# Performance work log

Hardware: AMD Instinct MI355X
Metric: run time of the kernel (lower is better)

## Reference

```python
import jax, jax.numpy as jnp
import numpy as np

B, N0, D0 = 256, 64, 128
N1, D1 = 64, 128


def setup_inputs() -> dict:
    key = jax.random.key(0)
    k1, k2 = jax.random.split(key)
    x = jax.random.normal(k1, (B, N0, D0), dtype=jnp.float32)
    # kaiming_normal_ (fan_in mode): fan_in = N0 * D0 * D1 for a [N1,N0,D0,D1] tensor
    std = np.sqrt(2.0 / (N0 * D0 * D1)).astype(np.float32)
    W = jax.random.normal(k2, (N1, N0, D0, D1), dtype=jnp.float32) * std
    b = jnp.zeros((N1, N0, 1), dtype=jnp.float32)
    return {"x": x, "W": W, "b": b}


def reference(x, W, b):
    u = jnp.einsum('bji,kjiz->bkjz', x, W)  # [B, N1, N0, D1]
    # c[b, n1, i] = sum_{k,j} u[b,n1,i,j] * u[b,n1,k,j] = u[b,n1,i,:] . sum_k u[b,n1,k,:]
    s = jnp.sum(u, axis=-2)                      # [B, N1, D1]
    c = jnp.einsum('bkjz,bkz->bkj', u, s)        # [B, N1, N0]
    c = c[..., None] / jnp.sqrt(jnp.asarray(u.shape[-1], dtype=u.dtype))
    c = jax.nn.softmax(c, axis=1)                # softmax over N1 (absolute axis 1)
    c = c + b
    return jnp.sum(u * c, axis=-2)               # [B, N1, D1]
```

## Files before the change

kernel.cpp:

```cpp
#include <hip/hip_runtime.h>
#include <hip/hip_bf16.h>
#include <cstdint>


#define BB 256
#define NN0 64
#define DD0 128
#define NN1 64
#define DD1 128

typedef __attribute__((ext_vector_type(8))) short bf16x8;
typedef __attribute__((ext_vector_type(4))) float f32x4;
typedef __attribute__((ext_vector_type(4))) ushort u16x4;

__device__ __forceinline__ ushort f2bf(float f) {
  uint32_t b = __float_as_uint(f);
  b += 0x7FFFu + ((b >> 16) & 1u);
  return (ushort)(b >> 16);
}
__device__ __forceinline__ float bf2f(ushort h) {
  return __uint_as_float(((uint32_t)h) << 16);
}

__device__ __forceinline__ void gld_lds16(const void* g, void* l) {
  __builtin_amdgcn_global_load_lds(
      (const __attribute__((address_space(1))) void*)g,
      (__attribute__((address_space(3))) void*)l, 16, 0, 0);
}

__device__ __forceinline__ void bar_lgkm() {
  asm volatile("s_waitcnt lgkmcnt(0)" ::: "memory");
  __builtin_amdgcn_s_barrier();
  __builtin_amdgcn_sched_barrier(0);
}

__global__ __launch_bounds__(512) void px_cvt(
    const float* __restrict__ x, ushort* __restrict__ xbf)
{
  int i = blockIdx.x * 512 + threadIdx.x;
  const f32x4* src = reinterpret_cast<const f32x4*>(x) + i;
  f32x4 v = __builtin_nontemporal_load(src);
  ushort4 h;
  h.x = f2bf(v.x); h.y = f2bf(v.y); h.z = f2bf(v.z); h.w = f2bf(v.w);
  *reinterpret_cast<ushort4*>(xbf + (size_t)i * 4) = h;
}

__global__ __launch_bounds__(512, 4) void k1_gemm(
    const ushort* __restrict__ xbf, const float* __restrict__ W,
    ushort* __restrict__ u)
{
  __shared__ __align__(16) char lds[81920];
  char* Alds = lds;
  char* Bl[2] = { lds + 65536, lds + 73728 };

  const int q = blockIdx.x;
  const int local = q >> 3;
  const int n0 = (q & 7) * 8 + (local >> 6);
  const int n1 = local & 63;
  const int t = threadIdx.x;
  const int lane = t & 63, wave = t >> 6;
  const int wm = wave >> 1, wn = wave & 1;

  const ushort* xb = xbf + n0 * DD0;
  const float* Wb = W + ((size_t)n1 * NN0 + n0) * (DD0 * DD1);
  ushort* ub = u + ((size_t)n1 * 8192 + (size_t)n0 * 128);

  f32x4 acc[4][4];
#pragma unroll
  for (int a = 0; a < 4; ++a)
#pragma unroll
    for (int b = 0; b < 4; ++b) acc[a][b] = {0.f, 0.f, 0.f, 0.f};

  const int gd1 = t & 127, gkc = t >> 7;
  const int bbyte = (gd1 * 64 + gkc * 16) ^ ((gd1 & 3) << 4) ^ (((gd1 >> 2) & 1) << 6);
  float w0[8], w1[8];

#define LOADW(hh, ks)                                                         \
  {                                                                           \
    _Pragma("unroll")                                                         \
    for (int j = 0; j < 8; ++j)                                               \
      hh[j] = __builtin_nontemporal_load(                                     \
          Wb + (size_t)((ks) * 32 + gkc * 8 + j) * 128 + gd1);                \
  }
#define PACKB(bi, hh)                                                         \
  {                                                                           \
    uint32_t p0 = (uint32_t)f2bf(hh[0]) | ((uint32_t)f2bf(hh[1]) << 16);      \
    uint32_t p1 = (uint32_t)f2bf(hh[2]) | ((uint32_t)f2bf(hh[3]) << 16);      \
    uint32_t p2 = (uint32_t)f2bf(hh[4]) | ((uint32_t)f2bf(hh[5]) << 16);      \
    uint32_t p3 = (uint32_t)f2bf(hh[6]) | ((uint32_t)f2bf(hh[7]) << 16);      \
    *reinterpret_cast<uint4*>(Bl[bi] + bbyte) = make_uint4(p0, p1, p2, p3);   \
  }
#define MFMA_STEP(ks, bi)                                                     \
  {                                                                           \
    const int kb16 = (lane >> 4);                                             \
    const int ka = (ks) * 32 + kb16 * 8;                                      \
    bf16x8 af[4], bfr[4];                                                     \
    _Pragma("unroll")                                                         \
    for (int mf = 0; mf < 4; ++mf) {                                          \
      int row = wm * 64 + mf * 16 + (lane & 15);                              \
      int byte = (row * 256 + ka * 2) ^ ((row & 7) << 4);                     \
      af[mf] = *reinterpret_cast<const bf16x8*>(Alds + byte);                 \
    }                                                                         \
    _Pragma("unroll")                                                         \
    for (int nf = 0; nf < 4; ++nf) {                                          \
      int n = wn * 64 + nf * 16 + (lane & 15);                                \
      int byte = (n * 64 + kb16 * 16) ^ ((n & 3) << 4) ^ (((n >> 2) & 1) << 6); \
      bfr[nf] = *reinterpret_cast<const bf16x8*>(Bl[bi] + byte);              \
    }                                                                         \
    _Pragma("unroll")                                                         \
    for (int mf = 0; mf < 4; ++mf)                                            \
      _Pragma("unroll")                                                       \
      for (int nf = 0; nf < 4; ++nf)                                          \
        acc[mf][nf] = __builtin_amdgcn_mfma_f32_16x16x32_bf16(af[mf], bfr[nf], acc[mf][nf], 0, 0, 0); \
  }

#pragma unroll
  for (int s = 0; s < 8; ++s) {
    int seg = wave * 8 + s;
    int row = seg * 4 + (lane >> 4);
    int srcc = (lane & 15) ^ (row & 7);
    gld_lds16(xb + (size_t)row * 8192 + srcc * 8, Alds + seg * 1024);
  }
  __builtin_amdgcn_sched_barrier(0);
  LOADW(w0, 0);
  __builtin_amdgcn_sched_barrier(0);
  LOADW(w1, 1);
  __builtin_amdgcn_sched_barrier(0);
  PACKB(0, w0);
  LOADW(w0, 2);
  __builtin_amdgcn_sched_barrier(0);
  bar_lgkm();

  PACKB(1, w1);
  LOADW(w1, 3);
  __builtin_amdgcn_sched_barrier(0);
  MFMA_STEP(0, 0);
  bar_lgkm();

  PACKB(0, w0);
  __builtin_amdgcn_sched_barrier(0);
  MFMA_STEP(1, 1);
  bar_lgkm();

  PACKB(1, w1);
  __builtin_amdgcn_sched_barrier(0);
  MFMA_STEP(2, 0);
  bar_lgkm();

  MFMA_STEP(3, 1);

  bar_lgkm();
#pragma unroll
  for (int mf = 0; mf < 4; ++mf) {
#pragma unroll
    for (int nf = 0; nf < 4; ++nf) {
      int col = wn * 64 + nf * 16 + (lane & 15);
#pragma unroll
      for (int j = 0; j < 4; ++j) {
        int rr = wm * 64 + mf * 16 + (lane >> 4) * 4 + j;
        int byte = (rr * 256 + col * 2) ^ ((rr & 7) << 4);
        *reinterpret_cast<ushort*>(Alds + byte) = f2bf(acc[mf][nf][j]);
      }
    }
  }
  bar_lgkm();
#pragma unroll
  for (int ci = 0; ci < 8; ++ci) {
    int c = t + ci * 512;
    int rowl = c >> 4;
    int cb = (c & 15) * 16;
    int sbyte = (rowl * 256 + cb) ^ ((rowl & 7) << 4);
    uint4 v = *reinterpret_cast<uint4*>(Alds + sbyte);
    *reinterpret_cast<uint4*>(ub + (size_t)rowl * 524288 + cb / 2) = v;
  }
#undef LOADW
#undef PACKB
#undef MFMA_STEP
}

__global__ __launch_bounds__(256) void k2_logits(
    const ushort* __restrict__ u, float* __restrict__ logits)
{
  const int bid = gridDim.x - 1 - blockIdx.x;
  const ushort* up = u + (size_t)bid * 8192;
  const int t = threadIdx.x;

  __shared__ float part[8][128];
  __shared__ float sS[128];
  __shared__ float part2[256];

  {
    int d4 = (t & 31) * 4;
    int g = t >> 5;
    float4 a = {0, 0, 0, 0};
    for (int n0 = g * 8; n0 < g * 8 + 8; ++n0) {
      ushort4 v = *reinterpret_cast<const ushort4*>(up + n0 * 128 + d4);
      a.x += bf2f(v.x); a.y += bf2f(v.y); a.z += bf2f(v.z); a.w += bf2f(v.w);
    }
    *reinterpret_cast<float4*>(&part[g][d4]) = a;
  }
  __syncthreads();
  if (t < 128) {
    float s = 0;
#pragma unroll
    for (int g = 0; g < 8; ++g) s += part[g][t];
    sS[t] = s;
  }
  __syncthreads();
  {
    int n0 = t >> 2, qq = t & 3;
    float acc = 0;
#pragma unroll
    for (int j = 0; j < 32; j += 4) {
      int d = qq * 32 + j;
      ushort4 v = *reinterpret_cast<const ushort4*>(up + n0 * 128 + d);
      acc += bf2f(v.x) * sS[d] + bf2f(v.y) * sS[d + 1] + bf2f(v.z) * sS[d + 2] + bf2f(v.w) * sS[d + 3];
    }
    part2[t] = acc;
  }
  __syncthreads();
  if (t < 64) {
    float l = (part2[t * 4] + part2[t * 4 + 1] + part2[t * 4 + 2] + part2[t * 4 + 3]) * 0.08838834764831845f;
    logits[(size_t)bid * 64 + t] = l;
  }
}

__global__ __launch_bounds__(64) void k3_softmax(
    const float* __restrict__ logits, const float* __restrict__ bias,
    float* __restrict__ cc)
{
  const int b = blockIdx.x;
  const int t = threadIdx.x;
  __shared__ float L[64][64];
  const float* lp = logits + (size_t)b * 4096;
  for (int i = 0; i < 64; ++i) L[i][t] = lp[i * 64 + t];
  __syncthreads();
  float m = -1e30f;
#pragma unroll
  for (int n1 = 0; n1 < 64; ++n1) m = fmaxf(m, L[n1][t]);
  float sum = 0.f;
#pragma unroll
  for (int n1 = 0; n1 < 64; ++n1) {
    float e = __expf(L[n1][t] - m);
    L[n1][t] = e;
    sum += e;
  }
  float inv = 1.0f / sum;
  float* cp = cc + (size_t)b * 4096;
  for (int n1 = 0; n1 < 64; ++n1)
    cp[n1 * 64 + t] = L[n1][t] * inv + bias[n1 * 64 + t];
}

__global__ __launch_bounds__(128) void k4_out(
    const ushort* __restrict__ u, const float* __restrict__ cc,
    float* __restrict__ out)
{
  const int bid = blockIdx.x;
  const ushort* up = u + (size_t)bid * 8192;
  const int t = threadIdx.x;
  __shared__ float cL[64];
  __shared__ float part[4][128];
  if (t < 64) cL[t] = cc[(size_t)bid * 64 + t];
  __syncthreads();
  int d4 = (t & 31) * 4, g = t >> 5;
  float4 a = {0, 0, 0, 0};
  for (int n0 = g * 16; n0 < g * 16 + 16; ++n0) {
    u16x4 v = __builtin_nontemporal_load(
        reinterpret_cast<const u16x4*>(up + n0 * 128 + d4));
    float c = cL[n0];
    a.x += bf2f(v.x) * c; a.y += bf2f(v.y) * c; a.z += bf2f(v.z) * c; a.w += bf2f(v.w) * c;
  }
  *reinterpret_cast<float4*>(&part[g][d4]) = a;
  __syncthreads();
  if (t < 128) {
    float r = part[0][t] + part[1][t] + part[2][t] + part[3][t];
    __builtin_nontemporal_store(r, &out[(size_t)bid * 128 + t]);
  }
}

extern "C" void kernel_launch(void* const* d_in, const int* in_sizes, int n_in,
                              void* d_out, int out_size, void* d_ws, size_t ws_size,
                              hipStream_t stream) {
  const float* x = (const float*)d_in[0];
  const float* W = (const float*)d_in[1];
  const float* bias = (const float*)d_in[2];
  float* out = (float*)d_out;

  ushort* u = (ushort*)d_ws;
  float* logits = (float*)((char*)d_ws + 268435456u);
  char* ccxbf = (char*)d_ws + 272629760u;
  ushort* xbf = (ushort*)ccxbf;
  float* cc = (float*)ccxbf;

  hipLaunchKernelGGL(px_cvt,     dim3(1024),     dim3(512), 0, stream, x, xbf);
  hipLaunchKernelGGL(k1_gemm,    dim3(4096),     dim3(512), 0, stream, xbf, W, u);
  hipLaunchKernelGGL(k2_logits,  dim3(BB * NN1), dim3(256), 0, stream, u, logits);
  hipLaunchKernelGGL(k3_softmax, dim3(BB),       dim3(64),  0, stream, logits, bias, cc);
  hipLaunchKernelGGL(k4_out,     dim3(BB * NN1), dim3(128), 0, stream, u, cc, out);
}
```

Baseline: 192.7 us.

## Fuse logits, softmax and output reduction into one per-batch kernel

Replaces three kernels (logits, softmax over N1, weighted output sum) with a single kernel that runs one 512-thread block per batch element. Each wave handles 8 n1 rows, computes column sums and logits with a shuffle-transpose reduction, then does the softmax over n1 in shared memory and the output sum. This removes two launches and the logits and cc round trips through global memory. In exchange the grid drops to 256 blocks, which may underfill the GPU, each block reads the u slab three times, and the 64-float register array adds register pressure.

Result: faster. 183.1 us (-5.0%).

```diff
diff --git a/kernel.cpp b/kernel.cpp
--- a/kernel.cpp
+++ b/kernel.cpp
@@ -11,7 +11,6 @@
 
 typedef __attribute__((ext_vector_type(8))) short bf16x8;
 typedef __attribute__((ext_vector_type(4))) float f32x4;
-typedef __attribute__((ext_vector_type(4))) ushort u16x4;
 
 __device__ __forceinline__ ushort f2bf(float f) {
   uint32_t b = __float_as_uint(f);
@@ -178,103 +177,104 @@
 #undef MFMA_STEP
 }
 
-__global__ __launch_bounds__(256) void k2_logits(
-    const ushort* __restrict__ u, float* __restrict__ logits)
-{
-  const int bid = gridDim.x - 1 - blockIdx.x;
-  const ushort* up = u + (size_t)bid * 8192;
-  const int t = threadIdx.x;
-
-  __shared__ float part[8][128];
-  __shared__ float sS[128];
-  __shared__ float part2[256];
-
-  {
-    int d4 = (t & 31) * 4;
-    int g = t >> 5;
-    float4 a = {0, 0, 0, 0};
-    for (int n0 = g * 8; n0 < g * 8 + 8; ++n0) {
-      ushort4 v = *reinterpret_cast<const ushort4*>(up + n0 * 128 + d4);
-      a.x += bf2f(v.x); a.y += bf2f(v.y); a.z += bf2f(v.z); a.w += bf2f(v.w);
-    }
-    *reinterpret_cast<float4*>(&part[g][d4]) = a;
-  }
-  __syncthreads();
-  if (t < 128) {
-    float s = 0;
-#pragma unroll
-    for (int g = 0; g < 8; ++g) s += part[g][t];
-    sS[t] = s;
-  }
-  __syncthreads();
-  {
-    int n0 = t >> 2, qq = t & 3;
-    float acc = 0;
-#pragma unroll
-    for (int j = 0; j < 32; j += 4) {
-      int d = qq * 32 + j;
-      ushort4 v = *reinterpret_cast<const ushort4*>(up + n0 * 128 + d);
-      acc += bf2f(v.x) * sS[d] + bf2f(v.y) * sS[d + 1] + bf2f(v.z) * sS[d + 2] + bf2f(v.w) * sS[d + 3];
-    }
-    part2[t] = acc;
-  }
-  __syncthreads();
-  if (t < 64) {
-    float l = (part2[t * 4] + part2[t * 4 + 1] + part2[t * 4 + 2] + part2[t * 4 + 3]) * 0.08838834764831845f;
-    logits[(size_t)bid * 64 + t] = l;
-  }
-}
-
-__global__ __launch_bounds__(64) void k3_softmax(
-    const float* __restrict__ logits, const float* __restrict__ bias,
-    float* __restrict__ cc)
+__global__ __launch_bounds__(512, 1) void k234_fused(
+    const ushort* __restrict__ u, const float* __restrict__ bias,
+    float* __restrict__ out)
 {
   const int b = blockIdx.x;
+  const ushort* ub = u + (size_t)b * 524288;
   const int t = threadIdx.x;
-  __shared__ float L[64][64];
-  const float* lp = logits + (size_t)b * 4096;
-  for (int i = 0; i < 64; ++i) L[i][t] = lp[i * 64 + t];
+  const int lane = t & 63, w = t >> 6;
+
+  __shared__ float cL[64][65];
+  __shared__ float red[2][8][64];
+
+#pragma unroll 1
+  for (int i = 0; i < 8; ++i) {
+    const int n1 = w * 8 + i;
+    const ushort* row = ub + n1 * 8192 + lane * 2;
+    float s0 = 0.f, s1 = 0.f;
+#pragma unroll
+    for (int n0 = 0; n0 < 64; ++n0) {
+      uint32_t v = *reinterpret_cast<const uint32_t*>(row + n0 * 128);
+      s0 += bf2f((ushort)(v & 0xffff));
+      s1 += bf2f((ushort)(v >> 16));
+    }
+    float p[64];
+#pragma unroll
+    for (int n0 = 0; n0 < 64; ++n0) {
+      uint32_t v = *reinterpret_cast<const uint32_t*>(row + n0 * 128);
+      p[n0] = bf2f((ushort)(v & 0xffff)) * s0 + bf2f((ushort)(v >> 16)) * s1;
+    }
+#pragma unroll
+    for (int s2 = 0; s2 < 6; ++s2) {
+      const int kb = (lane >> s2) & 1;
+#pragma unroll
+      for (int j = 0; j < (64 >> (s2 + 1)); ++j) {
+        float a = p[2 * j], b2 = p[2 * j + 1];
+        float mine = kb ? b2 : a;
+        float send = kb ? a : b2;
+        p[j] = mine + __shfl_xor(send, 1 << s2, 64);
+      }
+    }
+    cL[n1][lane] = p[0] * 0.08838834764831845f;
+  }
   __syncthreads();
-  float m = -1e30f;
-#pragma unroll
-  for (int n1 = 0; n1 < 64; ++n1) m = fmaxf(m, L[n1][t]);
-  float sum = 0.f;
-#pragma unroll
-  for (int n1 = 0; n1 < 64; ++n1) {
-    float e = __expf(L[n1][t] - m);
-    L[n1][t] = e;
-    sum += e;
-  }
-  float inv = 1.0f / sum;
-  float* cp = cc + (size_t)b * 4096;
-  for (int n1 = 0; n1 < 64; ++n1)
-    cp[n1 * 64 + t] = L[n1][t] * inv + bias[n1 * 64 + t];
-}
-
-__global__ __launch_bounds__(128) void k4_out(
-    const ushort* __restrict__ u, const float* __restrict__ cc,
-    float* __restrict__ out)
-{
-  const int bid = blockIdx.x;
-  const ushort* up = u + (size_t)bid * 8192;
-  const int t = threadIdx.x;
-  __shared__ float cL[64];
-  __shared__ float part[4][128];
-  if (t < 64) cL[t] = cc[(size_t)bid * 64 + t];
+
+  {
+    const int g = t >> 6, n0 = t & 63;
+    float pm = -1e30f;
+#pragma unroll
+    for (int j = 0; j < 8; ++j) pm = fmaxf(pm, cL[g * 8 + j][n0]);
+    red[0][g][n0] = pm;
+    __syncthreads();
+    if (g == 0) {
+      float m = red[0][0][n0];
+#pragma unroll
+      for (int j = 1; j < 8; ++j) m = fmaxf(m, red[0][j][n0]);
+      red[0][0][n0] = m;
+    }
+    __syncthreads();
+    const float m = red[0][0][n0];
+    float ps = 0.f;
+#pragma unroll
+    for (int j = 0; j < 8; ++j) {
+      float e = __expf(cL[g * 8 + j][n0] - m);
+      cL[g * 8 + j][n0] = e;
+      ps += e;
+    }
+    red[1][g][n0] = ps;
+    __syncthreads();
+    if (g == 0) {
+      float sm = 0.f;
+#pragma unroll
+      for (int j = 0; j < 8; ++j) sm += red[1][j][n0];
+      red[1][0][n0] = 1.0f / sm;
+    }
+    __syncthreads();
+    const float inv = red[1][0][n0];
+#pragma unroll
+    for (int j = 0; j < 8; ++j) {
+      int n1 = g * 8 + j;
+      cL[n1][n0] = cL[n1][n0] * inv + bias[n1 * 64 + n0];
+    }
+  }
   __syncthreads();
-  int d4 = (t & 31) * 4, g = t >> 5;
-  float4 a = {0, 0, 0, 0};
-  for (int n0 = g * 16; n0 < g * 16 + 16; ++n0) {
-    u16x4 v = __builtin_nontemporal_load(
-        reinterpret_cast<const u16x4*>(up + n0 * 128 + d4));
-    float c = cL[n0];
-    a.x += bf2f(v.x) * c; a.y += bf2f(v.y) * c; a.z += bf2f(v.z) * c; a.w += bf2f(v.w) * c;
-  }
-  *reinterpret_cast<float4*>(&part[g][d4]) = a;
-  __syncthreads();
-  if (t < 128) {
-    float r = part[0][t] + part[1][t] + part[2][t] + part[3][t];
-    __builtin_nontemporal_store(r, &out[(size_t)bid * 128 + t]);
+
+#pragma unroll 1
+  for (int i = 0; i < 8; ++i) {
+    const int n1 = w * 8 + i;
+    const ushort* row = ub + n1 * 8192 + lane * 2;
+    float o0 = 0.f, o1 = 0.f;
+#pragma unroll
+    for (int n0 = 0; n0 < 64; ++n0) {
+      uint32_t v = *reinterpret_cast<const uint32_t*>(row + n0 * 128);
+      float c = cL[n1][n0];
+      o0 += bf2f((ushort)(v & 0xffff)) * c;
+      o1 += bf2f((ushort)(v >> 16)) * c;
+    }
+    float2 o = make_float2(o0, o1);
+    *reinterpret_cast<float2*>(out + (size_t)b * 8192 + n1 * 128 + lane * 2) = o;
   }
 }
 
@@ -287,14 +287,9 @@
   float* out = (float*)d_out;
 
   ushort* u = (ushort*)d_ws;
-  float* logits = (float*)((char*)d_ws + 268435456u);
-  char* ccxbf = (char*)d_ws + 272629760u;
-  ushort* xbf = (ushort*)ccxbf;
-  float* cc = (float*)ccxbf;
-
-  hipLaunchKernelGGL(px_cvt,     dim3(1024),     dim3(512), 0, stream, x, xbf);
-  hipLaunchKernelGGL(k1_gemm,    dim3(4096),     dim3(512), 0, stream, xbf, W, u);
-  hipLaunchKernelGGL(k2_logits,  dim3(BB * NN1), dim3(256), 0, stream, u, logits);
-  hipLaunchKernelGGL(k3_softmax, dim3(BB),       dim3(64),  0, stream, logits, bias, cc);
-  hipLaunchKernelGGL(k4_out,     dim3(BB * NN1), dim3(128), 0, stream, u, cc, out);
-}
+  ushort* xbf = (ushort*)((char*)d_ws + 268435456u);
+
+  hipLaunchKernelGGL(px_cvt,     dim3(1024), dim3(512), 0, stream, x, xbf);
+  hipLaunchKernelGGL(k1_gemm,    dim3(4096), dim3(512), 0, stream, xbf, W, u);
+  hipLaunchKernelGGL(k234_fused, dim3(BB),   dim3(512), 0, stream, u, bias, out);
+}
```
